# Optimization experiments

Hardware: AMD Instinct MI355X
Metric: run time of the kernel (lower is better)

The kernel has to match this reference:

```python
import jax, jax.numpy as jnp
import numpy as np

B, T, H = 64, 2048, 256
NEG_INF = -10.0 ** 10  # matches torch code's -10**10 pad value


def setup_inputs() -> dict:
    key = jax.random.key(0)
    k1, k2, k3, k4, k5 = jax.random.split(key, 5)
    questions = jax.random.normal(k1, (B, T, H), dtype=jnp.float32)
    questions_lens = jax.random.randint(k2, (B,), 1, T + 1)  # lengths in [1, T]
    W = jax.random.normal(k3, (H, H), dtype=jnp.float32) * (1.0 / np.sqrt(H))
    b = jax.random.normal(k4, (H,), dtype=jnp.float32) * 0.02
    v = jax.random.normal(k5, (H,), dtype=jnp.float32) * (1.0 / np.sqrt(H))
    return {"questions": questions, "questions_lens": questions_lens, "W": W, "b": b, "v": v}


def reference(questions, questions_lens, W, b, v):
    # energy[b,t] = v . (W @ q[b,t] + b)  -- batched instead of per-token loop
    # = (q @ W^T) @ v + (b . v)
    energies = jnp.einsum('bth,h->bt', jnp.einsum('bth,kh->btk', questions, W) + b, v)
    t_idx = jnp.arange(questions.shape[1])  # [T]
    mask = t_idx[None, :] < questions_lens[:, None]  # [B,T] valid positions
    energies = jnp.where(mask, energies, NEG_INF)
    return jax.nn.softmax(energies, axis=1)
```

## Files before the change

kernel.cpp:

```cpp
#include <hip/hip_runtime.h>

constexpr int B_ = 64;
constexpr int T_ = 2048;
constexpr int H_ = 256;
constexpr float NEGINF = -1e10f;

__global__ __launch_bounds__(256) void prep1_kernel(
    const float* __restrict__ W, const float* __restrict__ bias,
    const float* __restrict__ v, float* __restrict__ partial,
    float* __restrict__ cptr) {
  const int h = threadIdx.x;
  const int j = blockIdx.x;
  float acc = 0.f;
#pragma unroll
  for (int kk = 0; kk < 4; ++kk) {
    const int k = j * 4 + kk;
    acc += v[k] * W[k * H_ + h];
  }
  partial[j * H_ + h] = acc;
  if (j == 0 && h == 0) {
    float cc = 0.f;
#pragma unroll 8
    for (int k = 0; k < H_; ++k) cc += v[k] * bias[k];
    *cptr = cc;
  }
}

__global__ __launch_bounds__(256) void prep2_kernel(
    const float* __restrict__ partial, float* __restrict__ u) {
  const int h = threadIdx.x;
  float acc = 0.f;
#pragma unroll
  for (int j = 0; j < 64; ++j) acc += partial[j * H_ + h];
  u[h] = acc;
}

constexpr int TOK_PER_BLOCK = 128;

__global__ __launch_bounds__(256) void energy_kernel(
    const float* __restrict__ q, const int* __restrict__ lens,
    const float* __restrict__ u, const float* __restrict__ cptr,
    float* __restrict__ e) {
  const int chunks_per_row = T_ / TOK_PER_BLOCK;
  const int bb = blockIdx.x / chunks_per_row;
  const int t0 = (blockIdx.x % chunks_per_row) * TOK_PER_BLOCK;
  const int wave = threadIdx.x >> 6;
  const int lane = threadIdx.x & 63;
  const int len = lens[bb];
  const float c = *cptr;
  const float4 uv = reinterpret_cast<const float4*>(u)[lane];
  const float4* qrow =
      reinterpret_cast<const float4*>(q) + (size_t)bb * T_ * (H_ / 4);
  float* erow = e + (size_t)bb * T_;

  for (int i = wave; i < TOK_PER_BLOCK; i += 4) {
    const int t = t0 + i;
    if (t < len) {
      const float4 qv = qrow[(size_t)t * (H_ / 4) + lane];
      float s = qv.x * uv.x + qv.y * uv.y + qv.z * uv.z + qv.w * uv.w;
#pragma unroll
      for (int off = 32; off > 0; off >>= 1) s += __shfl_xor(s, off);
      if (lane == 0) erow[t] = s + c;
    } else {
      if (lane == 0) erow[t] = NEGINF;
    }
  }
}

__global__ __launch_bounds__(256) void softmax_kernel(
    const float* __restrict__ e, float* __restrict__ out) {
  const int bb = blockIdx.x;
  const int tid = threadIdx.x;
  const int wave = tid >> 6;
  const int lane = tid & 63;
  const float* erow = e + (size_t)bb * T_;
  float* orow = out + (size_t)bb * T_;

  float vals[T_ / 256];
  float m = NEGINF;
#pragma unroll
  for (int i = 0; i < T_ / 256; ++i) {
    vals[i] = erow[i * 256 + tid];
    m = fmaxf(m, vals[i]);
  }
#pragma unroll
  for (int off = 32; off > 0; off >>= 1) m = fmaxf(m, __shfl_xor(m, off));

  __shared__ float sm[4];
  __shared__ float ssum[4];
  if (lane == 0) sm[wave] = m;
  __syncthreads();
  m = fmaxf(fmaxf(sm[0], sm[1]), fmaxf(sm[2], sm[3]));

  float s = 0.f;
#pragma unroll
  for (int i = 0; i < T_ / 256; ++i) {
    vals[i] = expf(vals[i] - m);
    s += vals[i];
  }
#pragma unroll
  for (int off = 32; off > 0; off >>= 1) s += __shfl_xor(s, off);
  if (lane == 0) ssum[wave] = s;
  __syncthreads();
  s = ssum[0] + ssum[1] + ssum[2] + ssum[3];
  const float inv = 1.f / s;
#pragma unroll
  for (int i = 0; i < T_ / 256; ++i) orow[i * 256 + tid] = vals[i] * inv;
}

extern "C" void kernel_launch(void* const* d_in, const int* in_sizes, int n_in,
                              void* d_out, int out_size, void* d_ws,
                              size_t ws_size, hipStream_t stream) {
  const float* q = (const float*)d_in[0];
  const int* lens = (const int*)d_in[1];
  const float* W = (const float*)d_in[2];
  const float* bias = (const float*)d_in[3];
  const float* v = (const float*)d_in[4];
  float* out = (float*)d_out;

  char* ws = (char*)d_ws;
  float* partial = (float*)ws;
  float* u = (float*)(ws + 64 * H_ * sizeof(float));
  float* c = (float*)(ws + 64 * H_ * sizeof(float) + H_ * sizeof(float));
  float* e = (float*)(ws + 131072);

  prep1_kernel<<<dim3(64), dim3(256), 0, stream>>>(W, bias, v, partial, c);
  prep2_kernel<<<dim3(1), dim3(256), 0, stream>>>(partial, u);
  energy_kernel<<<dim3(B_ * (T_ / TOK_PER_BLOCK)), dim3(256), 0, stream>>>(
      q, lens, u, c, e);
  softmax_kernel<<<dim3(B_), dim3(256), 0, stream>>>(e, out);
}
```

Before: 202.6 us.

## Fuse u reduction into energy kernel, drop bias constant, restructure token tiling

Removes the second prep kernel: the energy kernel now sums the four partial vectors itself, and the prep kernel shrinks to 4 blocks of 64 rows each. The constant bias·v term is dropped, which is valid because softmax is shift invariant. The energy kernel is retiled so each block handles 256 tokens, with 8 threads per token each holding 8 float4 of u, and a short 3-step shuffle reduction. Blocks lying entirely beyond the row length now exit early after writing the pad value. The aim is to cut one launch and the full-wave reductions, at the cost of extra register pressure and redundant partial sums in every block.

```diff
diff --git a/kernel.cpp b/kernel.cpp
--- a/kernel.cpp
+++ b/kernel.cpp
@@ -5,66 +5,85 @@
 constexpr int H_ = 256;
 constexpr float NEGINF = -1e10f;
 
-__global__ __launch_bounds__(256) void prep1_kernel(
-    const float* __restrict__ W, const float* __restrict__ bias,
-    const float* __restrict__ v, float* __restrict__ partial,
-    float* __restrict__ cptr) {
+__global__ __launch_bounds__(256) void prep_kernel(
+    const float* __restrict__ W, const float* __restrict__ v,
+    float* __restrict__ partial) {
   const int h = threadIdx.x;
   const int j = blockIdx.x;
   float acc = 0.f;
-#pragma unroll
-  for (int kk = 0; kk < 4; ++kk) {
-    const int k = j * 4 + kk;
-    acc += v[k] * W[k * H_ + h];
+#pragma unroll 8
+  for (int kk = 0; kk < 64; ++kk) {
+    const int k = j * 64 + kk;
+    acc = fmaf(v[k], W[k * H_ + h], acc);
   }
   partial[j * H_ + h] = acc;
-  if (j == 0 && h == 0) {
-    float cc = 0.f;
-#pragma unroll 8
-    for (int k = 0; k < H_; ++k) cc += v[k] * bias[k];
-    *cptr = cc;
-  }
 }
 
-__global__ __launch_bounds__(256) void prep2_kernel(
-    const float* __restrict__ partial, float* __restrict__ u) {
-  const int h = threadIdx.x;
-  float acc = 0.f;
-#pragma unroll
-  for (int j = 0; j < 64; ++j) acc += partial[j * H_ + h];
-  u[h] = acc;
-}
-
-constexpr int TOK_PER_BLOCK = 128;
-
 __global__ __launch_bounds__(256) void energy_kernel(
-    const float* __restrict__ q, const int* __restrict__ lens,
-    const float* __restrict__ u, const float* __restrict__ cptr,
+    const float4* __restrict__ q4, const int* __restrict__ lens,
+    const float4* __restrict__ p4,
     float* __restrict__ e) {
-  const int chunks_per_row = T_ / TOK_PER_BLOCK;
-  const int bb = blockIdx.x / chunks_per_row;
-  const int t0 = (blockIdx.x % chunks_per_row) * TOK_PER_BLOCK;
-  const int wave = threadIdx.x >> 6;
-  const int lane = threadIdx.x & 63;
+  const int bb = blockIdx.y;
+  const int t0 = blockIdx.x * 256;
   const int len = lens[bb];
-  const float c = *cptr;
-  const float4 uv = reinterpret_cast<const float4*>(u)[lane];
-  const float4* qrow =
-      reinterpret_cast<const float4*>(q) + (size_t)bb * T_ * (H_ / 4);
+  const int tid = threadIdx.x;
   float* erow = e + (size_t)bb * T_;
 
-  for (int i = wave; i < TOK_PER_BLOCK; i += 4) {
-    const int t = t0 + i;
+  if (t0 >= len) {
+    erow[t0 + tid] = NEGINF;
+    return;
+  }
+
+  const int tg = tid >> 3;
+  const int c4 = tid & 7;
+
+  float4 uf[8];
+#pragma unroll
+  for (int hh = 0; hh < 8; ++hh) {
+    float4 s = p4[hh * 8 + c4];
+#pragma unroll
+    for (int j = 1; j < 4; ++j) {
+      const float4 t = p4[j * 64 + hh * 8 + c4];
+      s.x += t.x; s.y += t.y; s.z += t.z; s.w += t.w;
+    }
+    uf[hh] = s;
+  }
+
+  const float4* qbase =
+      q4 + ((size_t)bb * T_ + t0 + tg) * (H_ / 4) + c4;
+
+  float acc[8];
+#pragma unroll
+  for (int i = 0; i < 8; ++i) acc[i] = 0.f;
+
+#pragma unroll
+  for (int i = 0; i < 8; ++i) {
+    const int t = t0 + tg + 32 * i;
     if (t < len) {
-      const float4 qv = qrow[(size_t)t * (H_ / 4) + lane];
-      float s = qv.x * uv.x + qv.y * uv.y + qv.z * uv.z + qv.w * uv.w;
+      const float4* qp = qbase + (size_t)i * 32 * (H_ / 4);
 #pragma unroll
-      for (int off = 32; off > 0; off >>= 1) s += __shfl_xor(s, off);
-      if (lane == 0) erow[t] = s + c;
-    } else {
-      if (lane == 0) erow[t] = NEGINF;
+      for (int hh = 0; hh < 8; ++hh) {
+        const float4 qv = qp[hh * 8];
+        acc[i] = fmaf(qv.x, uf[hh].x, acc[i]);
+        acc[i] = fmaf(qv.y, uf[hh].y, acc[i]);
+        acc[i] = fmaf(qv.z, uf[hh].z, acc[i]);
+        acc[i] = fmaf(qv.w, uf[hh].w, acc[i]);
+      }
     }
   }
+
+#pragma unroll
+  for (int off = 1; off < 8; off <<= 1) {
+#pragma unroll
+    for (int i = 0; i < 8; ++i) acc[i] += __shfl_xor(acc[i], off);
+  }
+
+  float val = 0.f;
+#pragma unroll
+  for (int k = 0; k < 8; ++k)
+    if (c4 == k) val = acc[k];
+  const int t = t0 + tg + 32 * c4;
+  erow[t] = (t < len) ? val : NEGINF;
 }
 
 __global__ __launch_bounds__(256) void softmax_kernel(
@@ -114,19 +133,15 @@
   const float* q = (const float*)d_in[0];
   const int* lens = (const int*)d_in[1];
   const float* W = (const float*)d_in[2];
-  const float* bias = (const float*)d_in[3];
   const float* v = (const float*)d_in[4];
   float* out = (float*)d_out;
 
   char* ws = (char*)d_ws;
   float* partial = (float*)ws;
-  float* u = (float*)(ws + 64 * H_ * sizeof(float));
-  float* c = (float*)(ws + 64 * H_ * sizeof(float) + H_ * sizeof(float));
-  float* e = (float*)(ws + 131072);
+  float* e = (float*)(ws + 8192);
 
-  prep1_kernel<<<dim3(64), dim3(256), 0, stream>>>(W, bias, v, partial, c);
-  prep2_kernel<<<dim3(1), dim3(256), 0, stream>>>(partial, u);
-  energy_kernel<<<dim3(B_ * (T_ / TOK_PER_BLOCK)), dim3(256), 0, stream>>>(
-      q, lens, u, c, e);
+  prep_kernel<<<dim3(4), dim3(256), 0, stream>>>(W, v, partial);
+  energy_kernel<<<dim3(T_ / 256, B_), dim3(256), 0, stream>>>(
+      (const float4*)q, lens, (const float4*)partial, e);
   softmax_kernel<<<dim3(B_), dim3(256), 0, stream>>>(e, out);
 }
```

After: 192.3 us. 5.1% less time.
